# Kernel optimization log

Measured on AMD Instinct MI355X. Metric: run time of the kernel, lower is better.

Reference implementation:

```python
import jax, jax.numpy as jnp
import numpy as np

# iRPE contextual+transposed, method=PRODUCT, rpe config ratio=1.9
ALPHA, BETA, GAMMA = 1.9, 3.8, 15.2
BETA_INT = int(BETA)            # 3
S = 2 * BETA_INT + 1            # 7
NUM_BUCKETS = S * S             # 49
B, H, D = 8, 8, 64
HEIGHT = WIDTH = 32
L = HEIGHT * WIDTH              # 1024, skip = L - height*width = 0


def _piecewise_index(rp):
    # numpy port of torch piecewise_index (no-grad, precomputed constant)
    rp = np.asarray(rp)
    rp_abs = np.abs(rp)
    safe = np.maximum(rp_abs.astype(np.float64), ALPHA)  # avoid log(0) under mask
    y = ALPHA + np.log(safe / ALPHA) / np.log(GAMMA / ALPHA) * (BETA - ALPHA)
    y = np.minimum(np.round(y), BETA)                    # round then clip(max=beta)
    out = np.where(rp_abs <= ALPHA, np.round(rp.astype(np.float64)), np.sign(rp) * y)
    return out.astype(np.int64)                          # trunc toward zero (+-3.8 -> +-3)


def _rp_bucket_product(height, width):
    pos = np.stack(np.meshgrid(np.arange(height), np.arange(width), indexing='ij'), -1)
    pos = pos.reshape(-1, 2)                             # (L, 2)
    diff = pos[:, None, :] - pos[None, :, :]             # (L, L, 2)
    r = _piecewise_index(diff[:, :, 0]) + BETA_INT
    c = _piecewise_index(diff[:, :, 1]) + BETA_INT
    return (r * S + c).astype(np.int32)                  # values in [0, 49)


def setup_inputs() -> dict:
    key = jax.random.key(0)
    k1, k2 = jax.random.split(key)
    x = jax.random.normal(k1, (B, H, L, D), dtype=jnp.float32)
    lookup_table_weight = jax.random.normal(k2, (H, D, NUM_BUCKETS), dtype=jnp.float32) * 0.02
    rp_bucket = jnp.asarray(_rp_bucket_product(HEIGHT, WIDTH))  # (L, L) int32 constant
    return {"x": x, "lookup_table_weight": lookup_table_weight, "rp_bucket": rp_bucket}


def reference(x, lookup_table_weight, rp_bucket):
    # x: (B, H, L, D); lookup_table_weight: (H, D, K); rp_bucket: (L, L) int
    # lt[b,h,l,k] = sum_d x[b,h,l,d] * W[h,d,k]
    lt = jnp.einsum('bhld,hdk->bhlk', x, lookup_table_weight)  # (B, H, L, K) small
    Lq = rp_bucket.shape[0]
    row = jnp.arange(Lq)[:, None]                              # (L, 1)
    # out[b,h,i,j] = lt[b,h,i,rp_bucket[i,j]] -- the big irregular gather
    return lt[:, :, row, rp_bucket]                            # (B, H, L, L)
```

## Files before the change

### kernel.cpp

```cpp
#include <hip/hip_runtime.h>


constexpr int cL = 1024;
constexpr int cD = 64;
constexpr int cK = 49;
constexpr int IG = 4;
constexpr int BG = 16;

__global__ __launch_bounds__(256, 4) void irpe_fused(
    const float* __restrict__ x,
    const float* __restrict__ W,
    const int*   __restrict__ bucket,
    float*       __restrict__ out)
{
    __shared__ float xs[BG * IG][cD];
    __shared__ float lts[BG * IG * cK];

    const int gid  = blockIdx.x;
    const int igrp = gid >> 2;
    const int bhg  = gid & 3;
    const int i0   = igrp * IG;
    const int bh0  = bhg * BG;
    const int tid  = threadIdx.x;
    const int lane = tid & 63;
    const int w    = tid >> 6;

    const float4* x4 = (const float4*)x;
    #pragma unroll
    for (int rr = 0; rr < 4; ++rr) {
        const int idx = rr * 256 + tid;
        const int row = idx >> 4;
        const int d4  = idx & 15;
        const int lhb = row >> 2;
        const int li  = row & 3;
        float4 v = x4[((size_t)(bh0 + lhb) * cL + (i0 + li)) * (cD / 4) + d4];
        ((float4*)xs[row])[d4] = v;
    }

    int4 bkt[IG * 4];
    #pragma unroll
    for (int t = 0; t < IG * 4; ++t) {
        const int li = t >> 2;
        const int jc = t & 3;
        bkt[t] = ((const int4*)(bucket + (size_t)(i0 + li) * cL + jc * 256))[lane];
    }

    __syncthreads();

    for (int p = tid; p < BG * IG * cK; p += 256) {
        const int row = p / cK;
        const int k   = p - row * cK;
        const int lhb = row >> 2;
        const int h   = lhb & 7;
        const float* wp = W + (size_t)h * cD * cK + k;
        const float* xr = xs[row];
        float acc = 0.0f;
        #pragma unroll
        for (int d = 0; d < cD; ++d)
            acc = fmaf(xr[d], wp[d * cK], acc);
        lts[p] = acc;
    }
    __syncthreads();

    #pragma unroll
    for (int q = 0; q < 4; ++q) {
        const int lhb = w * 4 + q;
        float4* pb = (float4*)(out + ((size_t)(bh0 + lhb) * cL + i0) * cL);
        const float* lbase = lts + lhb * (IG * cK);
        #pragma unroll 4
        for (int t = 0; t < IG * 4; ++t) {
            const int li = t >> 2;
            const float* lrow = lbase + li * cK;
            const int4 bk = bkt[t];
            float4 o;
            o.x = lrow[bk.x];
            o.y = lrow[bk.y];
            o.z = lrow[bk.z];
            o.w = lrow[bk.w];
            pb[t * 64 + lane] = o;
        }
    }
}

extern "C" void kernel_launch(void* const* d_in, const int* in_sizes, int n_in,
                              void* d_out, int out_size, void* d_ws, size_t ws_size,
                              hipStream_t stream) {
    const float* x      = (const float*)d_in[0];
    const float* W      = (const float*)d_in[1];
    const int*   bucket = (const int*)d_in[2];
    float*       out    = (float*)d_out;

    const int grid = (cL / IG) * (64 / BG);
    irpe_fused<<<grid, 256, 0, stream>>>(x, W, bucket, out);
}
```

Measured before the change: 347.2 us.

## Halve bh group per block, swizzle block order, and use nontemporal loads/stores

Reduces each block's batch-head group from 16 to 8 and remaps block IDs so neighbouring blocks cover different row groups. Bucket indices are loaded inside the gather loop instead of being held in registers, and launch bounds are raised for more occupancy. Nontemporal loads and stores are used for x and the large output write so the output stream does not pollute the caches. The trade-off is that bucket rows are now read twice as many times across blocks and the matmul loop is unrolled less.

```diff
diff --git a/kernel.cpp b/kernel.cpp
--- a/kernel.cpp
+++ b/kernel.cpp
@@ -5,80 +5,74 @@
 constexpr int cD = 64;
 constexpr int cK = 49;
 constexpr int IG = 4;
-constexpr int BG = 16;
+constexpr int BG = 8;
+constexpr int ROWS = IG * BG;
 
-__global__ __launch_bounds__(256, 4) void irpe_fused(
+typedef float vf4 __attribute__((ext_vector_type(4)));
+
+__global__ __launch_bounds__(256, 8) void irpe_fused(
     const float* __restrict__ x,
     const float* __restrict__ W,
     const int*   __restrict__ bucket,
     float*       __restrict__ out)
 {
-    __shared__ float xs[BG * IG][cD];
-    __shared__ float lts[BG * IG * cK];
+    __shared__ float xs[ROWS][cD];
+    __shared__ float lts[ROWS * cK];
 
     const int gid  = blockIdx.x;
-    const int igrp = gid >> 2;
-    const int bhg  = gid & 3;
+    const int k8   = gid >> 8;
+    const int c    = gid & 255;
+    const int igrp = ((c & 31) << 3) + k8;
+    const int bhg  = c >> 5;
     const int i0   = igrp * IG;
     const int bh0  = bhg * BG;
     const int tid  = threadIdx.x;
     const int lane = tid & 63;
     const int w    = tid >> 6;
 
-    const float4* x4 = (const float4*)x;
+    const vf4* x4 = (const vf4*)x;
     #pragma unroll
-    for (int rr = 0; rr < 4; ++rr) {
-        const int idx = rr * 256 + tid;
+    for (int r = 0; r < 2; ++r) {
+        const int idx = r * 256 + tid;
         const int row = idx >> 4;
         const int d4  = idx & 15;
         const int lhb = row >> 2;
         const int li  = row & 3;
-        float4 v = x4[((size_t)(bh0 + lhb) * cL + (i0 + li)) * (cD / 4) + d4];
-        ((float4*)xs[row])[d4] = v;
+        ((vf4*)xs[row])[d4] = __builtin_nontemporal_load(
+            &x4[((size_t)(bh0 + lhb) * cL + (i0 + li)) * (cD / 4) + d4]);
     }
-
-    int4 bkt[IG * 4];
-    #pragma unroll
-    for (int t = 0; t < IG * 4; ++t) {
-        const int li = t >> 2;
-        const int jc = t & 3;
-        bkt[t] = ((const int4*)(bucket + (size_t)(i0 + li) * cL + jc * 256))[lane];
-    }
-
     __syncthreads();
 
-    for (int p = tid; p < BG * IG * cK; p += 256) {
+    for (int p = tid; p < ROWS * cK; p += 256) {
         const int row = p / cK;
         const int k   = p - row * cK;
-        const int lhb = row >> 2;
-        const int h   = lhb & 7;
+        const int h   = row >> 2;
         const float* wp = W + (size_t)h * cD * cK + k;
         const float* xr = xs[row];
         float acc = 0.0f;
-        #pragma unroll
+        #pragma unroll 8
         for (int d = 0; d < cD; ++d)
             acc = fmaf(xr[d], wp[d * cK], acc);
         lts[p] = acc;
     }
     __syncthreads();
 
-    #pragma unroll
-    for (int q = 0; q < 4; ++q) {
-        const int lhb = w * 4 + q;
-        float4* pb = (float4*)(out + ((size_t)(bh0 + lhb) * cL + i0) * cL);
-        const float* lbase = lts + lhb * (IG * cK);
-        #pragma unroll 4
-        for (int t = 0; t < IG * 4; ++t) {
-            const int li = t >> 2;
-            const float* lrow = lbase + li * cK;
-            const int4 bk = bkt[t];
-            float4 o;
-            o.x = lrow[bk.x];
-            o.y = lrow[bk.y];
-            o.z = lrow[bk.z];
-            o.w = lrow[bk.w];
-            pb[t * 64 + lane] = o;
-        }
+    const int4* bpt = (const int4*)bucket + (size_t)i0 * (cL / 4);
+    vf4* p0 = (vf4*)out + ((size_t)(bh0 + 2 * w    ) * cL + i0) * (cL / 4);
+    vf4* p1 = (vf4*)out + ((size_t)(bh0 + 2 * w + 1) * cL + i0) * (cL / 4);
+    const float* l0 = lts + (2 * w    ) * (IG * cK);
+    const float* l1 = lts + (2 * w + 1) * (IG * cK);
+    #pragma unroll 4
+    for (int t = 0; t < 16; ++t) {
+        const int li = t >> 2;
+        const int4 bk = bpt[t * 64 + lane];
+        const float* r0 = l0 + li * cK;
+        const float* r1 = l1 + li * cK;
+        vf4 o0, o1;
+        o0.x = r0[bk.x]; o0.y = r0[bk.y]; o0.z = r0[bk.z]; o0.w = r0[bk.w];
+        o1.x = r1[bk.x]; o1.y = r1[bk.y]; o1.z = r1[bk.z]; o1.w = r1[bk.w];
+        __builtin_nontemporal_store(o0, &p0[t * 64 + lane]);
+        __builtin_nontemporal_store(o1, &p1[t * 64 + lane]);
     }
 }
 
```

Result: faster. 322.2 us (-7.2%).
